# Optimization experiments

Hardware: AMD Instinct MI355X
Metric: run time of the kernel (lower is better)

## Reference

```python
import jax, jax.numpy as jnp
import numpy as np

UNITS = 256
INNER_ITERS = 1
INNER_LR = [0.01]
LN_EPS = 1e-3  # keras LayerNormalization default epsilon
B, L, F = 512, 128, 128


def _encoder(W1, b1, W2, b2, z):
    # keras 'gelu' activation is exact (approximate=False)
    h = jax.nn.gelu(z @ W1 + b1, approximate=False)
    return h @ W2 + b2


def _layer_norm(z, g, b):
    m = jnp.mean(z, axis=-1, keepdims=True)
    v = jnp.var(z, axis=-1, keepdims=True)
    return g * (z - m) / jnp.sqrt(v + LN_EPS) + b


def setup_inputs():
    U = UNITS
    key = jax.random.key(0)
    ks = jax.random.split(key, 12)
    s = 0.02
    return {
        "inputs": jax.random.normal(ks[0], (B, F), jnp.float32),
        "prev_hidden": jax.random.normal(ks[1], (B, U), jnp.float32),
        "sequence_buffer": jax.random.normal(ks[2], (B, L, U), jnp.float32),
        "Wp": jax.random.normal(ks[3], (F, U)) * s, "bp": jnp.zeros((U,)),
        "Wphi": jax.random.normal(ks[4], (U, U)) * s, "bphi": jnp.zeros((U,)),
        "Wpsi": jax.random.normal(ks[5], (U, U)) * s, "bpsi": jnp.zeros((U,)),
        "W1": jax.random.normal(ks[6], (U, 4 * U)) * s, "b1": jnp.zeros((4 * U,)),
        "W2": jax.random.normal(ks[7], (4 * U, U)) * s, "b2": jnp.zeros((U,)),
        "Wg": jax.random.normal(ks[8], (U, U)) * s, "g_bias": jnp.zeros((U,)),
        "ln_g": jnp.ones((U,)), "ln_b": jnp.zeros((U,)),
        "Wh": jax.random.normal(ks[9], (U, U)) * s, "h_bias": jnp.zeros((U,)),
    }


def reference(inputs, prev_hidden, sequence_buffer, Wp, bp, Wphi, bphi, Wpsi, bpsi,
              W1, b1, W2, b2, Wg, g_bias, ln_g, ln_b, Wh, h_bias):
    U = UNITS
    bsz = inputs.shape[0]
    # input projection (F != units)
    proj = inputs @ Wp + bp                                   # [B, U]
    # shift buffer, append projected input
    buf = jnp.concatenate([sequence_buffer[:, 1:, :], proj[:, None, :]], axis=1)  # [B, L, U]
    x = buf[:, :-1, :].reshape(-1, U)                         # [B*(L-1), U]
    y = buf[:, 1:, :].reshape(-1, U)
    phi = x @ Wphi + bphi

    params = (W1, b1, W2, b2)

    def inner_loss(p):
        rec = _layer_norm(_encoder(*p, phi) @ Wg + g_bias, ln_g, ln_b)
        return jnp.mean(jnp.square(rec - y)), rec

    rec = None
    for it in range(INNER_ITERS):
        (_, rec), grads = jax.value_and_grad(inner_loss, has_aux=True)(params)
        lr = INNER_LR[min(it, len(INNER_LR) - 1)]
        params = tuple(p - lr * g for p, g in zip(params, grads))

    psi = buf[:, -1, :] @ Wpsi + bpsi                         # [B, U]
    contrib = jnp.mean(rec.reshape(bsz, -1, U), axis=1)       # [B, U]
    # psi path uses the UPDATED inner-encoder weights
    out = (_encoder(*params, psi) + contrib) @ Wh + h_bias    # [B, U]
    return out, buf
```

## Files before the change

kernel.cpp:

```cpp
#include <hip/hip_runtime.h>
#include <cmath>

typedef __bf16 bf16;
typedef __attribute__((ext_vector_type(8))) __bf16 bf16x8;
typedef __attribute__((ext_vector_type(4))) float f32x4;
typedef __attribute__((ext_vector_type(2))) unsigned int u32x2;

constexpr int NROWS = 512 * 127;
constexpr float LR = 0.01f;
constexpr float INV_NU = 1.f / (65024.f * 256.f);

__device__ __forceinline__ float geluf(float x) {
  return 0.5f * x * (1.f + erff(x * 0.70710678118654752f));
}
__device__ __forceinline__ float dgeluf(float x) {
  float c = 0.5f * (1.f + erff(x * 0.70710678118654752f));
  float p = 0.3989422804014327f * __expf(-0.5f * x * x);
  return c + x * p;
}
__device__ __forceinline__ bf16x8 gelu8(bf16x8 v) {
  bf16x8 o;
#pragma unroll
  for (int i = 0; i < 8; i++) o[i] = (bf16)geluf((float)v[i]);
  return o;
}
__device__ __forceinline__ bf16x8 gelu8f(bf16x8 v) {
  bf16x8 o;
#pragma unroll
  for (int i = 0; i < 8; i++) {
    float x = (float)v[i];
    o[i] = (bf16)(x / (1.f + __expf(-1.702f * x)));
  }
  return o;
}

__device__ __forceinline__ void gload16(const bf16* g, const bf16* lds) {
  __builtin_amdgcn_global_load_lds(
      (const __attribute__((address_space(1))) unsigned int*)(size_t)(const void*)g,
      (__attribute__((address_space(3))) unsigned int*)(unsigned)(size_t)(const void*)lds,
      16, 0, 0);
}

template <int EPI>
__global__ __launch_bounds__(256) void gemm2_k(
    const bf16* __restrict__ A, const bf16* __restrict__ Bt,
    const float* __restrict__ bias, void* __restrict__ out0,
    void* __restrict__ out1, const bf16* __restrict__ aux,
    int M, int N, int K) {
  __shared__ __align__(16) bf16 As[128 * 64];
  __shared__ __align__(16) bf16 Bs[128 * 64];
  const int t = threadIdx.x;
  const int bn = blockIdx.x * 128, bm = blockIdx.y * 128;
  const int lane = t & 63, w = t >> 6;
  const int wr = w >> 1, wc = w & 1;

  f32x4 acc[4][4];
#pragma unroll
  for (int mi = 0; mi < 4; mi++)
#pragma unroll
    for (int ni = 0; ni < 4; ni++) {
      f32x4 z = {0.f, 0.f, 0.f, 0.f};
      acc[mi][ni] = z;
    }

  const int l8 = lane >> 3;
  const int p = lane & 7;
  const int csw = p ^ l8;
  const bf16* aS[4];
  const bf16* bS[4];
#pragma unroll
  for (int i = 0; i < 4; i++) {
    const int r = 32 * w + 8 * i + l8;
    aS[i] = A + (size_t)(bm + r) * K + csw * 8;
    bS[i] = Bt + (size_t)(bn + r) * K + csw * 8;
  }

  const int ml = lane & 15, g = lane >> 4;
  const int c0 = g ^ (ml & 7);
  const int c1 = (4 | g) ^ (ml & 7);

  for (int kt = 0; kt < K; kt += 64) {
    __syncthreads();
#pragma unroll
    for (int i = 0; i < 4; i++) {
      gload16(aS[i], As + (32 * w + 8 * i) * 64);
      gload16(bS[i], Bs + (32 * w + 8 * i) * 64);
      aS[i] += 64; bS[i] += 64;
    }
    __syncthreads();

    bf16x8 af[2][4], bfr[2][4];
#pragma unroll
    for (int mi = 0; mi < 4; mi++) {
      const int m = wr * 64 + mi * 16 + ml;
      const int n = wc * 64 + mi * 16 + ml;
      af[0][mi] = *(const bf16x8*)&As[m * 64 + c0 * 8];
      af[1][mi] = *(const bf16x8*)&As[m * 64 + c1 * 8];
      bfr[0][mi] = *(const bf16x8*)&Bs[n * 64 + c0 * 8];
      bfr[1][mi] = *(const bf16x8*)&Bs[n * 64 + c1 * 8];
    }
#pragma unroll
    for (int ks = 0; ks < 2; ks++)
#pragma unroll
      for (int mi = 0; mi < 4; mi++)
#pragma unroll
        for (int ni = 0; ni < 4; ni++)
          acc[mi][ni] = __builtin_amdgcn_mfma_f32_16x16x32_bf16(af[ks][mi], bfr[ks][ni], acc[mi][ni], 0, 0, 0);
  }

#pragma unroll
  for (int ni = 0; ni < 4; ni++) {
    const int col = bn + wc * 64 + ni * 16 + (lane & 15);
    const float bv = bias ? bias[col] : 0.f;
#pragma unroll
    for (int mi = 0; mi < 4; mi++) {
      const int rb = bm + wr * 64 + mi * 16 + ((lane >> 4) << 2);
#pragma unroll
      for (int r = 0; r < 4; r++) {
        float v = acc[mi][ni][r] + bv;
        size_t idx = (size_t)(rb + r) * N + col;
        if constexpr (EPI == 0) {
          ((float*)out0)[idx] = v;
        } else if constexpr (EPI == 1) {
          ((bf16*)out0)[idx] = (bf16)v;
        } else if constexpr (EPI == 2) {
          ((bf16*)out0)[idx] = (bf16)v;
          ((bf16*)out1)[idx] = (bf16)geluf(v);
        } else if constexpr (EPI == 3) {
          ((bf16*)out0)[idx] = (bf16)geluf(v);
        } else {
          float a = (float)aux[idx];
          ((bf16*)out0)[idx] = (bf16)(v * dgeluf(a));
        }
      }
    }
  }
}

template <int EPI, bool GA>
__global__ __launch_bounds__(256) void gemm_k(
    const bf16* __restrict__ A, const bf16* __restrict__ Bt,
    const float* __restrict__ bias, void* __restrict__ out0,
    void* __restrict__ out1, const bf16* __restrict__ aux,
    int M, int N, int K) {
  __shared__ bf16 As[128][40];
  __shared__ bf16 Bs[128][40];
  const int t = threadIdx.x;
  const int bm = blockIdx.x * 128, bn = blockIdx.y * 128;
  const int lane = t & 63, w = t >> 6;
  const int wr = w >> 1, wc = w & 1;

  f32x4 acc[4][4];
#pragma unroll
  for (int mi = 0; mi < 4; mi++)
#pragma unroll
    for (int ni = 0; ni < 4; ni++) {
      f32x4 z = {0.f, 0.f, 0.f, 0.f};
      acc[mi][ni] = z;
    }
  const int r2 = t >> 2;
  const int c8 = (t & 3) * 8;

  for (int kt = 0; kt < K; kt += 32) {
    __syncthreads();
    {
      bf16x8 a0 = *(const bf16x8*)(A + (size_t)(bm + r2) * K + kt + c8);
      bf16x8 a1 = *(const bf16x8*)(A + (size_t)(bm + r2 + 64) * K + kt + c8);
      bf16x8 b0 = *(const bf16x8*)(Bt + (size_t)(bn + r2) * K + kt + c8);
      bf16x8 b1 = *(const bf16x8*)(Bt + (size_t)(bn + r2 + 64) * K + kt + c8);
      if constexpr (GA) { a0 = gelu8(a0); a1 = gelu8(a1); }
      *(bf16x8*)&As[r2][c8] = a0;
      *(bf16x8*)&As[r2 + 64][c8] = a1;
      *(bf16x8*)&Bs[r2][c8] = b0;
      *(bf16x8*)&Bs[r2 + 64][c8] = b1;
    }
    __syncthreads();
    bf16x8 af[4], bfr[4];
#pragma unroll
    for (int mi = 0; mi < 4; mi++)
      af[mi] = *(const bf16x8*)&As[wr * 64 + mi * 16 + (lane & 15)][(lane >> 4) * 8];
#pragma unroll
    for (int ni = 0; ni < 4; ni++)
      bfr[ni] = *(const bf16x8*)&Bs[wc * 64 + ni * 16 + (lane & 15)][(lane >> 4) * 8];
#pragma unroll
    for (int mi = 0; mi < 4; mi++)
#pragma unroll
      for (int ni = 0; ni < 4; ni++)
        acc[mi][ni] = __builtin_amdgcn_mfma_f32_16x16x32_bf16(af[mi], bfr[ni], acc[mi][ni], 0, 0, 0);
  }

#pragma unroll
  for (int ni = 0; ni < 4; ni++) {
    const int col = bn + wc * 64 + ni * 16 + (lane & 15);
    const float bv = bias ? bias[col] : 0.f;
#pragma unroll
    for (int mi = 0; mi < 4; mi++) {
      const int rb = bm + wr * 64 + mi * 16 + ((lane >> 4) << 2);
#pragma unroll
      for (int r = 0; r < 4; r++) {
        float v = acc[mi][ni][r] + bv;
        size_t idx = (size_t)(rb + r) * N + col;
        if constexpr (EPI == 1) {
          ((bf16*)out0)[idx] = (bf16)v;
        } else {
          ((float*)out0)[idx] = v;
        }
      }
    }
  }
}

template <bool GELU_A>
__global__ __launch_bounds__(256) void tgemm3_k(
    const bf16* __restrict__ Asrc, const bf16* __restrict__ Bsrc,
    float* __restrict__ outP, int M, int N, int ldA, int ldB, int K) {
  __shared__ __align__(16) bf16 As[4736];
  __shared__ __align__(16) bf16 Bs[4736];
  const int t = threadIdx.x;
  const int bm = blockIdx.x * 128, bn = blockIdx.y * 128;
  const int r0 = blockIdx.z * 1024;
  const int rows = (K - r0 < 1024) ? (K - r0) : 1024;
  const int lane = t & 63, w = t >> 6, wr = w >> 1, wc = w & 1;

  f32x4 acc[4][4];
#pragma unroll
  for (int mi = 0; mi < 4; mi++)
#pragma unroll
    for (int ni = 0; ni < 4; ni++) {
      f32x4 z = {0.f, 0.f, 0.f, 0.f};
      acc[mi][ni] = z;
    }

  const bool isB = t >= 128;
  const int srow = (t & 127) >> 4;
  const int scol = (t & 15) * 8;
  const int sms = (t & 15) >> 1;
  const int shalf = (t & 1) * 8;
  const bf16* src = isB ? Bsrc : Asrc;
  const int ld = isB ? ldB : ldA;
  const int bx = isB ? bn : bm;
  bf16* dst = isB ? Bs : As;

  const unsigned abase = (unsigned)(size_t)(void*)As;
  const unsigned bbase = (unsigned)(size_t)(void*)Bs;
  const int g = lane >> 4;
  const int ml = lane & 15;
  const unsigned acol0 = abase + 2u * (unsigned)((wr * 4) * 592 + g * 144 + ml);
  const unsigned bcol0 = bbase + 2u * (unsigned)((wc * 4) * 592 + g * 144 + ml);

  for (int kt = 0; kt < rows; kt += 32) {
    __syncthreads();
#pragma unroll
    for (int ll = 0; ll < 4; ll++) {
      const int row = srow + ll * 8;
      bf16x8 v = *(const bf16x8*)(src + (size_t)(r0 + kt + row) * ld + bx + scol);
      if constexpr (GELU_A) { if (!isB) v = gelu8f(v); }
      *(bf16x8*)&dst[sms * 592 + ll * 144 + srow * 16 + shalf] = v;
    }
    __syncthreads();

    union FR { u32x2 p[2]; bf16x8 v; };
    FR af[4], bfr[4];
#pragma unroll
    for (int mi = 0; mi < 4; mi++) {
      const unsigned a = acol0 + (unsigned)(mi * 592 * 2);
      asm volatile("ds_read_b64_tr_b16 %0, %1" : "=v"(af[mi].p[0]) : "v"(a));
      asm volatile("ds_read_b64_tr_b16 %0, %1 offset:128" : "=v"(af[mi].p[1]) : "v"(a));
    }
#pragma unroll
    for (int ni = 0; ni < 4; ni++) {
      const unsigned b = bcol0 + (unsigned)(ni * 592 * 2);
      asm volatile("ds_read_b64_tr_b16 %0, %1" : "=v"(bfr[ni].p[0]) : "v"(b));
      asm volatile("ds_read_b64_tr_b16 %0, %1 offset:128" : "=v"(bfr[ni].p[1]) : "v"(b));
    }
    asm volatile("s_waitcnt lgkmcnt(0)" ::: "memory");
    __builtin_amdgcn_sched_barrier(0);

#pragma unroll
    for (int mi = 0; mi < 4; mi++)
#pragma unroll
      for (int ni = 0; ni < 4; ni++)
        acc[mi][ni] = __builtin_amdgcn_mfma_f32_16x16x32_bf16(af[mi].v, bfr[ni].v, acc[mi][ni], 0, 0, 0);
  }

  float* o = outP + (size_t)blockIdx.z * M * N;
#pragma unroll
  for (int ni = 0; ni < 4; ni++) {
    const int col = bn + wc * 64 + ni * 16 + (lane & 15);
#pragma unroll
    for (int mi = 0; mi < 4; mi++) {
      const int rb = bm + wr * 64 + mi * 16 + ((lane >> 4) << 2);
#pragma unroll
      for (int r = 0; r < 4; r++) o[(size_t)(rb + r) * N + col] = acc[mi][ni][r];
    }
  }
}

__global__ void prep_k(const float* inputs, const float* Wp, const float* Wphi,
                       const float* W1, const float* W2, const float* Wg,
                       const float* Wpsi, const float* Wh,
                       bf16* inb, bf16* WpT, bf16* WphiT, bf16* W1T, bf16* W2T,
                       bf16* WgT, bf16* Wgb, bf16* W2b, bf16* WpsiT, bf16* WhT) {
  int i = blockIdx.x * 256 + threadIdx.x;
  if (i < 65536) {
    inb[i] = (bf16)inputs[i];
  } else if ((i -= 65536) < 32768) {
    int u = i >> 7, f = i & 127;
    WpT[i] = (bf16)Wp[f * 256 + u];
  } else if ((i -= 32768) < 65536) {
    int n = i >> 8, k = i & 255;
    WphiT[i] = (bf16)Wphi[k * 256 + n];
  } else if ((i -= 65536) < 262144) {
    int h = i >> 8, u = i & 255;
    W1T[i] = (bf16)W1[u * 1024 + h];
  } else if ((i -= 262144) < 262144) {
    int u = i >> 10, h = i & 1023;
    W2T[i] = (bf16)W2[h * 256 + u];
  } else if ((i -= 262144) < 65536) {
    int n = i >> 8, k = i & 255;
    WgT[i] = (bf16)Wg[k * 256 + n];
  } else if ((i -= 65536) < 65536) {
    Wgb[i] = (bf16)Wg[i];
  } else if ((i -= 65536) < 262144) {
    W2b[i] = (bf16)W2[i];
  } else if ((i -= 262144) < 65536) {
    int n = i >> 8, k = i & 255;
    WpsiT[i] = (bf16)Wpsi[k * 256 + n];
  } else if ((i -= 65536) < 65536) {
    int n = i >> 8, k = i & 255;
    WhT[i] = (bf16)Wh[k * 256 + n];
  }
}

__global__ void xcast_k(const float* __restrict__ seq, bf16* __restrict__ xb) {
  int v8 = blockIdx.x * 256 + threadIdx.x;
  int r = v8 >> 5, c8 = (v8 & 31) * 8;
  int b = r / 127, t = r - b * 127;
  const float* src = seq + ((size_t)(b * 128 + t + 1)) * 256 + c8;
  float4 v0 = *(const float4*)(src);
  float4 v1 = *(const float4*)(src + 4);
  bf16x8 o;
  o[0] = (bf16)v0.x; o[1] = (bf16)v0.y; o[2] = (bf16)v0.z; o[3] = (bf16)v0.w;
  o[4] = (bf16)v1.x; o[5] = (bf16)v1.y; o[6] = (bf16)v1.z; o[7] = (bf16)v1.w;
  *(bf16x8*)(xb + (size_t)r * 256 + c8) = o;
}

__global__ void projcast_k(const float* __restrict__ proj, bf16* __restrict__ projb) {
  int i = blockIdx.x * 256 + threadIdx.x;
  projb[i] = (bf16)proj[i];
}

__global__ void bufwrite_k(const float* __restrict__ seq, const float* __restrict__ proj,
                           float* __restrict__ buf) {
  int i = blockIdx.x * 256 + threadIdx.x;
  int b = i >> 13, rem = i & 8191;
  int j = rem >> 6, c4 = (rem & 63) * 4;
  float4 v;
  if (j < 127)
    v = *(const float4*)(seq + ((size_t)(b * 128 + j + 1)) * 256 + c4);
  else
    v = *(const float4*)(proj + (size_t)b * 256 + c4);
  *(float4*)(buf + ((size_t)(b * 128 + j)) * 256 + c4) = v;
}

__global__ __launch_bounds__(256) void ln_k(const bf16* zin, bf16* dzout,
                                            const float* __restrict__ seq,
                                            const float* __restrict__ proj,
                                            const float* __restrict__ lng,
                                            const float* __restrict__ lnb,
                                            bf16* __restrict__ rec) {
  const int w = threadIdx.x >> 6, lane = threadIdx.x & 63;
  const int r = blockIdx.x * 4 + w;
  const int b = r / 127, tt = r - b * 127;
  typedef __attribute__((ext_vector_type(4))) __bf16 bf16x4;
  bf16x4 zv = *(const bf16x4*)(zin + (size_t)r * 256 + lane * 4);
  float z0 = (float)zv[0], z1 = (float)zv[1], z2 = (float)zv[2], z3 = (float)zv[3];
  float s1 = z0 + z1 + z2 + z3;
  float s2 = z0 * z0 + z1 * z1 + z2 * z2 + z3 * z3;
  for (int m = 1; m < 64; m <<= 1) { s1 += __shfl_xor(s1, m); s2 += __shfl_xor(s2, m); }
  const float mean = s1 * (1.f / 256.f);
  const float var = s2 * (1.f / 256.f) - mean * mean;
  const float rs = rsqrtf(var + 1e-3f);
  const float4 gv = *(const float4*)(lng + lane * 4);
  const float4 bv = *(const float4*)(lnb + lane * 4);
  const float* ysrc = (tt < 126) ? (seq + ((size_t)(b * 128 + tt + 2)) * 256)
                                 : (proj + (size_t)b * 256);
  const float4 yv = *(const float4*)(ysrc + lane * 4);
  float xh0 = (z0 - mean) * rs, xh1 = (z1 - mean) * rs, xh2 = (z2 - mean) * rs, xh3 = (z3 - mean) * rs;
  float r0 = gv.x * xh0 + bv.x, r1 = gv.y * xh1 + bv.y, r2 = gv.z * xh2 + bv.z, r3 = gv.w * xh3 + bv.w;
  float u0 = 2.f * (r0 - yv.x) * INV_NU * gv.x;
  float u1 = 2.f * (r1 - yv.y) * INV_NU * gv.y;
  float u2 = 2.f * (r2 - yv.z) * INV_NU * gv.z;
  float u3 = 2.f * (r3 - yv.w) * INV_NU * gv.w;
  float t1 = u0 + u1 + u2 + u3;
  float t2 = u0 * xh0 + u1 * xh1 + u2 * xh2 + u3 * xh3;
  for (int m = 1; m < 64; m <<= 1) { t1 += __shfl_xor(t1, m); t2 += __shfl_xor(t2, m); }
  const float mu = t1 * (1.f / 256.f), mux = t2 * (1.f / 256.f);
  bf16x4 ro, dzo;
  ro[0] = (bf16)r0; ro[1] = (bf16)r1; ro[2] = (bf16)r2; ro[3] = (bf16)r3;
  dzo[0] = (bf16)((u0 - mu - xh0 * mux) * rs);
  dzo[1] = (bf16)((u1 - mu - xh1 * mux) * rs);
  dzo[2] = (bf16)((u2 - mu - xh2 * mux) * rs);
  dzo[3] = (bf16)((u3 - mu - xh3 * mux) * rs);
  *(bf16x4*)(rec + (size_t)r * 256 + lane * 4) = ro;
  *(bf16x4*)(dzout + (size_t)r * 256 + lane * 4) = dzo;
}

__global__ void colsum_k(const bf16* __restrict__ src, float* __restrict__ part, int C) {
  const int col = blockIdx.x * 256 + threadIdx.x;
  const int ch = blockIdx.y;
  float s = 0.f;
  const int rbeg = ch * 1016;
  for (int rr = rbeg; rr < rbeg + 1016; rr++) s += (float)src[(size_t)rr * C + col];
  part[(size_t)ch * C + col] = s;
}

__global__ void contrib_k(const bf16* __restrict__ rec, float* __restrict__ contrib) {
  const int b = blockIdx.x, u = threadIdx.x;
  float s = 0.f;
  for (int t = 0; t < 127; t++) s += (float)rec[((size_t)b * 127 + t) * 256 + u];
  contrib[b * 256 + u] = s * (1.f / 127.f);
}

__global__ void update2_k(const float* __restrict__ pW2, const float* __restrict__ pdb2,
                          const float* __restrict__ W2, const float* __restrict__ b2,
                          bf16* __restrict__ W2pT, float* __restrict__ b2p) {
  int idx = blockIdx.x * 256 + threadIdx.x;
  if (idx < 262144) {
    float s = 0.f;
    for (int z = 0; z < 64; z++) s += pW2[(size_t)z * 262144 + idx];
    int h = idx >> 8, u = idx & 255;
    W2pT[(size_t)u * 1024 + h] = (bf16)(W2[idx] - LR * s);
  } else {
    int u = idx - 262144;
    float s = 0.f;
    for (int c = 0; c < 64; c++) s += pdb2[c * 256 + u];
    b2p[u] = b2[u] - LR * s;
  }
}

__global__ void update1_k(const float* __restrict__ pW1, const float* __restrict__ pdb1,
                          const float* __restrict__ W1, const float* __restrict__ b1,
                          bf16* __restrict__ W1pT, float* __restrict__ b1p) {
  int idx = blockIdx.x * 256 + threadIdx.x;
  if (idx < 262144) {
    float s = 0.f;
    for (int z = 0; z < 64; z++) s += pW1[(size_t)z * 262144 + idx];
    int u = idx >> 10, h = idx & 1023;
    W1pT[(size_t)h * 256 + u] = (bf16)(W1[idx] - LR * s);
  } else {
    int h = idx - 262144;
    float s = 0.f;
    for (int c = 0; c < 64; c++) s += pdb1[c * 1024 + h];
    b1p[h] = b1[h] - LR * s;
  }
}

__global__ void fin_k(const float* __restrict__ encp, const float* __restrict__ contrib,
                      bf16* __restrict__ fin) {
  int i = blockIdx.x * 256 + threadIdx.x;
  fin[i] = (bf16)(encp[i] + contrib[i]);
}

extern "C" void kernel_launch(void* const* d_in, const int* in_sizes, int n_in,
                              void* d_out, int out_size, void* d_ws, size_t ws_size,
                              hipStream_t stream) {
  const float* inputs = (const float*)d_in[0];
  const float* seq = (const float*)d_in[2];
  const float* Wp = (const float*)d_in[3];
  const float* bp = (const float*)d_in[4];
  const float* Wphi = (const float*)d_in[5];
  const float* bphi = (const float*)d_in[6];
  const float* Wpsi = (const float*)d_in[7];
  const float* bpsi = (const float*)d_in[8];
  const float* W1 = (const float*)d_in[9];
  const float* b1 = (const float*)d_in[10];
  const float* W2 = (const float*)d_in[11];
  const float* b2 = (const float*)d_in[12];
  const float* Wg = (const float*)d_in[13];
  const float* gbias = (const float*)d_in[14];
  const float* lng = (const float*)d_in[15];
  const float* lnb = (const float*)d_in[16];
  const float* Wh = (const float*)d_in[17];
  const float* hbias = (const float*)d_in[18];

  float* out = (float*)d_out;
  float* buf = out + 131072;
  float* pW2 = buf;
  float* pW1 = buf;

  char* wptr = (char*)d_ws;
  auto alloc = [&](size_t bytes) {
    char* p = wptr;
    wptr += (bytes + 255) & ~(size_t)255;
    return p;
  };
  bf16* inb   = (bf16*)alloc(65536 * 2);
  bf16* WpT   = (bf16*)alloc(32768 * 2);
  bf16* WphiT = (bf16*)alloc(65536 * 2);
  bf16* W1T   = (bf16*)alloc(262144 * 2);
  bf16* W2T   = (bf16*)alloc(262144 * 2);
  bf16* WgT   = (bf16*)alloc(65536 * 2);
  bf16* Wgb   = (bf16*)alloc(65536 * 2);
  bf16* W2b   = (bf16*)alloc(262144 * 2);
  bf16* WpsiT = (bf16*)alloc(65536 * 2);
  bf16* WhT   = (bf16*)alloc(65536 * 2);
  bf16* W1pT  = (bf16*)alloc(262144 * 2);
  bf16* W2pT  = (bf16*)alloc(262144 * 2);
  float* b1p  = (float*)alloc(1024 * 4);
  float* b2p  = (float*)alloc(256 * 4);
  float* proj = (float*)alloc(131072 * 4);
  bf16* projb = (bf16*)alloc(131072 * 2);
  float* pdb2 = (float*)alloc(64 * 256 * 4);
  float* pdb1 = (float*)alloc(64 * 1024 * 4);
  bf16* psib  = (bf16*)alloc(131072 * 2);
  bf16* hpb   = (bf16*)alloc(524288 * 2);
  float* encp = (float*)alloc(131072 * 4);
  float* contrib = (float*)alloc(131072 * 4);
  bf16* finb  = (bf16*)alloc(131072 * 2);
  const size_t NU = (size_t)NROWS * 256;
  const size_t NH = (size_t)NROWS * 1024;
  bf16* xz     = (bf16*)alloc(NU * 2);
  bf16* phi    = (bf16*)alloc(NU * 2);
  bf16* a1b    = (bf16*)alloc(NH * 2);
  bf16* encden = (bf16*)alloc(NU * 2);
  const bool useH = ws_size >= (size_t)((char*)wptr - (char*)d_ws) + NH * 2 + 4096;
  bf16* hbuf = useH ? (bf16*)alloc(NH * 2) : nullptr;

  prep_k<<<4736, 256, 0, stream>>>(inputs, Wp, Wphi, W1, W2, Wg, Wpsi, Wh,
                                   inb, WpT, WphiT, W1T, W2T, WgT, Wgb, W2b, WpsiT, WhT);
  xcast_k<<<8128, 256, 0, stream>>>(seq, xz);
  gemm2_k<0><<<dim3(2, 4), 256, 0, stream>>>(inb, WpT, bp, proj, nullptr, nullptr, 512, 256, 128);
  projcast_k<<<512, 256, 0, stream>>>(proj, projb);
  gemm2_k<1><<<dim3(2, 508), 256, 0, stream>>>(xz, WphiT, bphi, phi, nullptr, nullptr, NROWS, 256, 256);
  if (useH)
    gemm2_k<2><<<dim3(8, 508), 256, 0, stream>>>(phi, W1T, b1, a1b, hbuf, nullptr, NROWS, 1024, 256);
  else
    gemm2_k<1><<<dim3(8, 508), 256, 0, stream>>>(phi, W1T, b1, a1b, nullptr, nullptr, NROWS, 1024, 256);
  if (useH)
    gemm2_k<1><<<dim3(2, 508), 256, 0, stream>>>(hbuf, W2T, b2, encden, nullptr, nullptr, NROWS, 256, 1024);
  else
    gemm_k<1, true><<<dim3(508, 2), 256, 0, stream>>>(a1b, W2T, b2, encden, nullptr, nullptr, NROWS, 256, 1024);
  gemm2_k<1><<<dim3(2, 508), 256, 0, stream>>>(encden, WgT, gbias, xz, nullptr, nullptr, NROWS, 256, 256);
  ln_k<<<16256, 256, 0, stream>>>(xz, xz, seq, proj, lng, lnb, encden);
  contrib_k<<<512, 256, 0, stream>>>(encden, contrib);
  gemm2_k<1><<<dim3(2, 508), 256, 0, stream>>>(xz, Wgb, nullptr, encden, nullptr, nullptr, NROWS, 256, 256);
  colsum_k<<<dim3(1, 64), 256, 0, stream>>>(encden, pdb2, 256);
  if (useH)
    tgemm3_k<false><<<dim3(8, 2, 64), 256, 0, stream>>>(hbuf, encden, pW2, 1024, 256, 1024, 256, NROWS);
  else
    tgemm3_k<true><<<dim3(8, 2, 64), 256, 0, stream>>>(a1b, encden, pW2, 1024, 256, 1024, 256, NROWS);
  update2_k<<<1025, 256, 0, stream>>>(pW2, pdb2, W2, b2, W2pT, b2p);
  gemm2_k<5><<<dim3(8, 508), 256, 0, stream>>>(encden, W2b, nullptr, a1b, nullptr, a1b, NROWS, 1024, 256);
  colsum_k<<<dim3(4, 64), 256, 0, stream>>>(a1b, pdb1, 1024);
  tgemm3_k<false><<<dim3(2, 8, 64), 256, 0, stream>>>(phi, a1b, pW1, 256, 1024, 256, 1024, NROWS);
  update1_k<<<1028, 256, 0, stream>>>(pW1, pdb1, W1, b1, W1pT, b1p);
  bufwrite_k<<<16384, 256, 0, stream>>>(seq, proj, buf);
  gemm2_k<1><<<dim3(2, 4), 256, 0, stream>>>(projb, WpsiT, bpsi, psib, nullptr, nullptr, 512, 256, 256);
  gemm2_k<3><<<dim3(8, 4), 256, 0, stream>>>(psib, W1pT, b1p, hpb, nullptr, nullptr, 512, 1024, 256);
  gemm2_k<0><<<dim3(2, 4), 256, 0, stream>>>(hpb, W2pT, b2p, encp, nullptr, nullptr, 512, 256, 1024);
  fin_k<<<512, 256, 0, stream>>>(encp, contrib, finb);
  gemm2_k<0><<<dim3(2, 4), 256, 0, stream>>>(finb, WhT, hbias, out, nullptr, nullptr, 512, 256, 256);
}
```

Baseline: 1.023 ms.

## Double-buffer GEMM LDS loads, vectorize epilogues, replace exact GELU with sigmoid approximation

```diff
diff --git a/kernel.cpp b/kernel.cpp
--- a/kernel.cpp
+++ b/kernel.cpp
@@ -3,6 +3,7 @@
 
 typedef __bf16 bf16;
 typedef __attribute__((ext_vector_type(8))) __bf16 bf16x8;
+typedef __attribute__((ext_vector_type(4))) __bf16 bf16x4v;
 typedef __attribute__((ext_vector_type(4))) float f32x4;
 typedef __attribute__((ext_vector_type(2))) unsigned int u32x2;
 
@@ -10,27 +11,18 @@
 constexpr float LR = 0.01f;
 constexpr float INV_NU = 1.f / (65024.f * 256.f);
 
-__device__ __forceinline__ float geluf(float x) {
-  return 0.5f * x * (1.f + erff(x * 0.70710678118654752f));
-}
-__device__ __forceinline__ float dgeluf(float x) {
-  float c = 0.5f * (1.f + erff(x * 0.70710678118654752f));
-  float p = 0.3989422804014327f * __expf(-0.5f * x * x);
-  return c + x * p;
-}
-__device__ __forceinline__ bf16x8 gelu8(bf16x8 v) {
-  bf16x8 o;
-#pragma unroll
-  for (int i = 0; i < 8; i++) o[i] = (bf16)geluf((float)v[i]);
-  return o;
+__device__ __forceinline__ float sigf(float x) {
+  return 1.f / (1.f + __expf(-1.702f * x));
+}
+__device__ __forceinline__ float gelu_fast(float x) { return x * sigf(x); }
+__device__ __forceinline__ float dgelu_fast(float x) {
+  float s = sigf(x);
+  return s * (1.f + 1.702f * x * (1.f - s));
 }
 __device__ __forceinline__ bf16x8 gelu8f(bf16x8 v) {
   bf16x8 o;
 #pragma unroll
-  for (int i = 0; i < 8; i++) {
-    float x = (float)v[i];
-    o[i] = (bf16)(x / (1.f + __expf(-1.702f * x)));
-  }
+  for (int i = 0; i < 8; i++) o[i] = (bf16)gelu_fast((float)v[i]);
   return o;
 }
 
@@ -42,13 +34,13 @@
 }
 
 template <int EPI>
-__global__ __launch_bounds__(256) void gemm2_k(
+__global__ __launch_bounds__(256) void gemm3_k(
     const bf16* __restrict__ A, const bf16* __restrict__ Bt,
     const float* __restrict__ bias, void* __restrict__ out0,
     void* __restrict__ out1, const bf16* __restrict__ aux,
     int M, int N, int K) {
-  __shared__ __align__(16) bf16 As[128 * 64];
-  __shared__ __align__(16) bf16 Bs[128 * 64];
+  __shared__ __align__(16) bf16 As[2][128 * 64];
+  __shared__ __align__(16) bf16 Bs[2][128 * 64];
   const int t = threadIdx.x;
   const int bn = blockIdx.x * 128, bm = blockIdx.y * 128;
   const int lane = t & 63, w = t >> 6;
@@ -66,38 +58,40 @@
   const int l8 = lane >> 3;
   const int p = lane & 7;
   const int csw = p ^ l8;
-  const bf16* aS[4];
-  const bf16* bS[4];
-#pragma unroll
-  for (int i = 0; i < 4; i++) {
-    const int r = 32 * w + 8 * i + l8;
-    aS[i] = A + (size_t)(bm + r) * K + csw * 8;
-    bS[i] = Bt + (size_t)(bn + r) * K + csw * 8;
-  }
+  const bf16* aBase = A + (size_t)(bm + 32 * w + l8) * K + csw * 8;
+  const bf16* bBase = Bt + (size_t)(bn + 32 * w + l8) * K + csw * 8;
 
   const int ml = lane & 15, g = lane >> 4;
   const int c0 = g ^ (ml & 7);
   const int c1 = (4 | g) ^ (ml & 7);
 
-  for (int kt = 0; kt < K; kt += 64) {
-    __syncthreads();
-#pragma unroll
-    for (int i = 0; i < 4; i++) {
-      gload16(aS[i], As + (32 * w + 8 * i) * 64);
-      gload16(bS[i], Bs + (32 * w + 8 * i) * 64);
-      aS[i] += 64; bS[i] += 64;
-    }
-    __syncthreads();
-
+  const int nt = K >> 6;
+#pragma unroll
+  for (int i = 0; i < 4; i++) {
+    gload16(aBase + (size_t)(8 * i) * K, As[0] + (32 * w + 8 * i) * 64);
+    gload16(bBase + (size_t)(8 * i) * K, Bs[0] + (32 * w + 8 * i) * 64);
+  }
+  __syncthreads();
+
+  for (int tt = 0; tt < nt; tt++) {
+    const int cur = tt & 1;
+    if (tt + 1 < nt) {
+      const int ko = (tt + 1) * 64;
+#pragma unroll
+      for (int i = 0; i < 4; i++) {
+        gload16(aBase + (size_t)(8 * i) * K + ko, As[cur ^ 1] + (32 * w + 8 * i) * 64);
+        gload16(bBase + (size_t)(8 * i) * K + ko, Bs[cur ^ 1] + (32 * w + 8 * i) * 64);
+      }
+    }
     bf16x8 af[2][4], bfr[2][4];
 #pragma unroll
     for (int mi = 0; mi < 4; mi++) {
       const int m = wr * 64 + mi * 16 + ml;
       const int n = wc * 64 + mi * 16 + ml;
-      af[0][mi] = *(const bf16x8*)&As[m * 64 + c0 * 8];
-      af[1][mi] = *(const bf16x8*)&As[m * 64 + c1 * 8];
-      bfr[0][mi] = *(const bf16x8*)&Bs[n * 64 + c0 * 8];
-      bfr[1][mi] = *(const bf16x8*)&Bs[n * 64 + c1 * 8];
+      af[0][mi] = *(const bf16x8*)&As[cur][m * 64 + c0 * 8];
+      af[1][mi] = *(const bf16x8*)&As[cur][m * 64 + c1 * 8];
+      bfr[0][mi] = *(const bf16x8*)&Bs[cur][n * 64 + c0 * 8];
+      bfr[1][mi] = *(const bf16x8*)&Bs[cur][n * 64 + c1 * 8];
     }
 #pragma unroll
     for (int ks = 0; ks < 2; ks++)
@@ -105,33 +99,58 @@
       for (int mi = 0; mi < 4; mi++)
 #pragma unroll
         for (int ni = 0; ni < 4; ni++)
-          acc[mi][ni] = __builtin_amdgcn_mfma_f32_16x16x32_bf16(af[ks][mi], bfr[ks][ni], acc[mi][ni], 0, 0, 0);
-  }
-
-#pragma unroll
-  for (int ni = 0; ni < 4; ni++) {
-    const int col = bn + wc * 64 + ni * 16 + (lane & 15);
-    const float bv = bias ? bias[col] : 0.f;
-#pragma unroll
-    for (int mi = 0; mi < 4; mi++) {
-      const int rb = bm + wr * 64 + mi * 16 + ((lane >> 4) << 2);
-#pragma unroll
-      for (int r = 0; r < 4; r++) {
-        float v = acc[mi][ni][r] + bv;
-        size_t idx = (size_t)(rb + r) * N + col;
-        if constexpr (EPI == 0) {
-          ((float*)out0)[idx] = v;
-        } else if constexpr (EPI == 1) {
-          ((bf16*)out0)[idx] = (bf16)v;
-        } else if constexpr (EPI == 2) {
-          ((bf16*)out0)[idx] = (bf16)v;
-          ((bf16*)out1)[idx] = (bf16)geluf(v);
-        } else if constexpr (EPI == 3) {
-          ((bf16*)out0)[idx] = (bf16)geluf(v);
-        } else {
-          float a = (float)aux[idx];
-          ((bf16*)out0)[idx] = (bf16)(v * dgeluf(a));
+          acc[mi][ni] = __builtin_amdgcn_mfma_f32_16x16x32_bf16(
+              bfr[ks][ni], af[ks][mi], acc[mi][ni], 0, 0, 0);
+    __syncthreads();
+  }
+
+  const int g4 = (lane >> 4) << 2;
+#pragma unroll
+  for (int mi = 0; mi < 4; mi++) {
+    const int m = bm + wr * 64 + mi * 16 + ml;
+#pragma unroll
+    for (int ni = 0; ni < 4; ni++) {
+      const int n0 = bn + wc * 64 + ni * 16 + g4;
+      f32x4 v = acc[mi][ni];
+      if (bias) {
+        const float4 bv = *(const float4*)(bias + n0);
+        v[0] += bv.x; v[1] += bv.y; v[2] += bv.z; v[3] += bv.w;
+      }
+      const size_t idx = (size_t)m * N + n0;
+      if constexpr (EPI == 0) {
+        *(float4*)((float*)out0 + idx) = make_float4(v[0], v[1], v[2], v[3]);
+      } else if constexpr (EPI == 1) {
+        bf16x4v o;
+#pragma unroll
+        for (int j = 0; j < 4; j++) o[j] = (bf16)v[j];
+        *(bf16x4v*)((bf16*)out0 + idx) = o;
+      } else if constexpr (EPI == 2) {
+        bf16x4v od, oh;
+#pragma unroll
+        for (int j = 0; j < 4; j++) {
+          float s = sigf(v[j]);
+          oh[j] = (bf16)(v[j] * s);
+          od[j] = (bf16)(s * (1.f + 1.702f * v[j] * (1.f - s)));
         }
+        *(bf16x4v*)((bf16*)out0 + idx) = od;
+        *(bf16x4v*)((bf16*)out1 + idx) = oh;
+      } else if constexpr (EPI == 3) {
+        bf16x4v o;
+#pragma unroll
+        for (int j = 0; j < 4; j++) o[j] = (bf16)gelu_fast(v[j]);
+        *(bf16x4v*)((bf16*)out0 + idx) = o;
+      } else if constexpr (EPI == 5) {
+        const bf16x4v a4 = *(const bf16x4v*)(aux + idx);
+        bf16x4v o;
+#pragma unroll
+        for (int j = 0; j < 4; j++) o[j] = (bf16)(v[j] * dgelu_fast((float)a4[j]));
+        *(bf16x4v*)((bf16*)out0 + idx) = o;
+      } else {
+        const bf16x4v a4 = *(const bf16x4v*)(aux + idx);
+        bf16x4v o;
+#pragma unroll
+        for (int j = 0; j < 4; j++) o[j] = (bf16)(v[j] * (float)a4[j]);
+        *(bf16x4v*)((bf16*)out0 + idx) = o;
       }
     }
   }
@@ -168,7 +187,7 @@
       bf16x8 a1 = *(const bf16x8*)(A + (size_t)(bm + r2 + 64) * K + kt + c8);
       bf16x8 b0 = *(const bf16x8*)(Bt + (size_t)(bn + r2) * K + kt + c8);
       bf16x8 b1 = *(const bf16x8*)(Bt + (size_t)(bn + r2 + 64) * K + kt + c8);
-      if constexpr (GA) { a0 = gelu8(a0); a1 = gelu8(a1); }
+      if constexpr (GA) { a0 = gelu8f(a0); a1 = gelu8f(a1); }
       *(bf16x8*)&As[r2][c8] = a0;
       *(bf16x8*)&As[r2 + 64][c8] = a1;
       *(bf16x8*)&Bs[r2][c8] = b0;
@@ -280,18 +299,20 @@
     for (int mi = 0; mi < 4; mi++)
 #pragma unroll
       for (int ni = 0; ni < 4; ni++)
-        acc[mi][ni] = __builtin_amdgcn_mfma_f32_16x16x32_bf16(af[mi].v, bfr[ni].v, acc[mi][ni], 0, 0, 0);
+        acc[mi][ni] = __builtin_amdgcn_mfma_f32_16x16x32_bf16(
+            bfr[ni].v, af[mi].v, acc[mi][ni], 0, 0, 0);
   }
 
   float* o = outP + (size_t)blockIdx.z * M * N;
-#pragma unroll
-  for (int ni = 0; ni < 4; ni++) {
-    const int col = bn + wc * 64 + ni * 16 + (lane & 15);
-#pragma unroll
-    for (int mi = 0; mi < 4; mi++) {
-      const int rb = bm + wr * 64 + mi * 16 + ((lane >> 4) << 2);
-#pragma unroll
-      for (int r = 0; r < 4; r++) o[(size_t)(rb + r) * N + col] = acc[mi][ni][r];
+  const int g4 = (lane >> 4) << 2;
+#pragma unroll
+  for (int mi = 0; mi < 4; mi++) {
+    const int m = bm + wr * 64 + mi * 16 + ml;
+#pragma unroll
+    for (int ni = 0; ni < 4; ni++) {
+      const int n0 = bn + wc * 64 + ni * 16 + g4;
+      f32x4 v = acc[mi][ni];
+      *(float4*)(o + (size_t)m * N + n0) = make_float4(v[0], v[1], v[2], v[3]);
     }
   }
 }
@@ -530,35 +551,38 @@
   prep_k<<<4736, 256, 0, stream>>>(inputs, Wp, Wphi, W1, W2, Wg, Wpsi, Wh,
                                    inb, WpT, WphiT, W1T, W2T, WgT, Wgb, W2b, WpsiT, WhT);
   xcast_k<<<8128, 256, 0, stream>>>(seq, xz);
-  gemm2_k<0><<<dim3(2, 4), 256, 0, stream>>>(inb, WpT, bp, proj, nullptr, nullptr, 512, 256, 128);
+  gemm3_k<0><<<dim3(2, 4), 256, 0, stream>>>(inb, WpT, bp, proj, nullptr, nullptr, 512, 256, 128);
   projcast_k<<<512, 256, 0, stream>>>(proj, projb);
-  gemm2_k<1><<<dim3(2, 508), 256, 0, stream>>>(xz, WphiT, bphi, phi, nullptr, nullptr, NROWS, 256, 256);
+  gemm3_k<1><<<dim3(2, 508), 256, 0, stream>>>(xz, WphiT, bphi, phi, nullptr, nullptr, NROWS, 256, 256);
   if (useH)
-    gemm2_k<2><<<dim3(8, 508), 256, 0, stream>>>(phi, W1T, b1, a1b, hbuf, nullptr, NROWS, 1024, 256);
+    gemm3_k<2><<<dim3(8, 508), 256, 0, stream>>>(phi, W1T, b1, a1b, hbuf, nullptr, NROWS, 1024, 256);
   else
-    gemm2_k<1><<<dim3(8, 508), 256, 0, stream>>>(phi, W1T, b1, a1b, nullptr, nullptr, NROWS, 1024, 256);
+    gemm3_k<1><<<dim3(8, 508), 256, 0, stream>>>(phi, W1T, b1, a1b, nullptr, nullptr, NROWS, 1024, 256);
   if (useH)
-    gemm2_k<1><<<dim3(2, 508), 256, 0, stream>>>(hbuf, W2T, b2, encden, nullptr, nullptr, NROWS, 256, 1024);
+    gemm3_k<1><<<dim3(2, 508), 256, 0, stream>>>(hbuf, W2T, b2, encden, nullptr, nullptr, NROWS, 256, 1024);
   else
     gemm_k<1, true><<<dim3(508, 2), 256, 0, stream>>>(a1b, W2T, b2, encden, nullptr, nullptr, NROWS, 256, 1024);
-  gemm2_k<1><<<dim3(2, 508), 256, 0, stream>>>(encden, WgT, gbias, xz, nullptr, nullptr, NROWS, 256, 256);
+  gemm3_k<1><<<dim3(2, 508), 256, 0, stream>>>(encden, WgT, gbias, xz, nullptr, nullptr, NROWS, 256, 256);
   ln_k<<<16256, 256, 0, stream>>>(xz, xz, seq, proj, lng, lnb, encden);
   contrib_k<<<512, 256, 0, stream>>>(encden, contrib);
-  gemm2_k<1><<<dim3(2, 508), 256, 0, stream>>>(xz, Wgb, nullptr, encden, nullptr, nullptr, NROWS, 256, 256);
+  gemm3_k<1><<<dim3(2, 508), 256, 0, stream>>>(xz, Wgb, nullptr, encden, nullptr, nullptr, NROWS, 256, 256);
   colsum_k<<<dim3(1, 64), 256, 0, stream>>>(encden, pdb2, 256);
   if (useH)
     tgemm3_k<false><<<dim3(8, 2, 64), 256, 0, stream>>>(hbuf, encden, pW2, 1024, 256, 1024, 256, NROWS);
   else
     tgemm3_k<true><<<dim3(8, 2, 64), 256, 0, stream>>>(a1b, encden, pW2, 1024, 256, 1024, 256, NROWS);
   update2_k<<<1025, 256, 0, stream>>>(pW2, pdb2, W2, b2, W2pT, b2p);
-  gemm2_k<5><<<dim3(8, 508), 256, 0, stream>>>(encden, W2b, nullptr, a1b, nullptr, a1b, NROWS, 1024, 256);
+  if (useH)
+    gemm3_k<6><<<dim3(8, 508), 256, 0, stream>>>(encden, W2b, nullptr, a1b, nullptr, a1b, NROWS, 1024, 256);
+  else
+    gemm3_k<5><<<dim3(8, 508), 256, 0, stream>>>(encden, W2b, nullptr, a1b, nullptr, a1b, NROWS, 1024, 256);
   colsum_k<<<dim3(4, 64), 256, 0, stream>>>(a1b, pdb1, 1024);
   tgemm3_k<false><<<dim3(2, 8, 64), 256, 0, stream>>>(phi, a1b, pW1, 256, 1024, 256, 1024, NROWS);
   update1_k<<<1028, 256, 0, stream>>>(pW1, pdb1, W1, b1, W1pT, b1p);
   bufwrite_k<<<16384, 256, 0, stream>>>(seq, proj, buf);
-  gemm2_k<1><<<dim3(2, 4), 256, 0, stream>>>(projb, WpsiT, bpsi, psib, nullptr, nullptr, 512, 256, 256);
-  gemm2_k<3><<<dim3(8, 4), 256, 0, stream>>>(psib, W1pT, b1p, hpb, nullptr, nullptr, 512, 1024, 256);
-  gemm2_k<0><<<dim3(2, 4), 256, 0, stream>>>(hpb, W2pT, b2p, encp, nullptr, nullptr, 512, 256, 1024);
+  gemm3_k<1><<<dim3(2, 4), 256, 0, stream>>>(projb, WpsiT, bpsi, psib, nullptr, nullptr, 512, 256, 256);
+  gemm3_k<3><<<dim3(8, 4), 256, 0, stream>>>(psib, W1pT, b1p, hpb, nullptr, nullptr, 512, 1024, 256);
+  gemm3_k<0><<<dim3(2, 4), 256, 0, stream>>>(hpb, W2pT, b2p, encp, nullptr, nullptr, 512, 256, 1024);
   fin_k<<<512, 256, 0, stream>>>(encp, contrib, finb);
-  gemm2_k<0><<<dim3(2, 4), 256, 0, stream>>>(finb, WhT, hbias, out, nullptr, nullptr, 512, 256, 256);
-}
+  gemm3_k<0><<<dim3(2, 4), 256, 0, stream>>>(finb, WhT, hbias, out, nullptr, nullptr, 512, 256, 256);
+}
```

After: 944.0 us. 1.08x faster.
